# Kernel tuning notes

Measured on AMD Instinct MI355X. Metric: run time of the kernel, lower is better.

## Reference

```python
import jax, jax.numpy as jnp
import numpy as np

N = 50000   # nodes
E = 800000  # directed edges
IN, H1, H2, OUT = 128, 64, 32, 40
K = 2       # SGConv hops


def setup_inputs() -> dict:
    key = jax.random.key(0)
    ks = jax.random.split(key, 8)
    x = jax.random.normal(ks[0], (N, IN), dtype=jnp.float32)
    edge_index = jax.random.randint(ks[1], (2, E), 0, N, dtype=jnp.int64)
    s = lambda k, shp, fan: jax.random.normal(k, shp, dtype=jnp.float32) / np.sqrt(fan)
    return {
        "x": x,
        "edge_index": edge_index,
        "W1": s(ks[2], (IN, H1), IN), "b1": jnp.zeros((H1,), jnp.float32),
        "W2": s(ks[3], (H1, H2), H1), "b2": jnp.zeros((H2,), jnp.float32),
        "Wf": s(ks[4], (H2, OUT), H2), "bf": jnp.zeros((OUT,), jnp.float32),
    }


def _gcn_norm(edge_index, num_nodes):
    # add self-loops, then norm = d^{-1/2}[src] * d^{-1/2}[dst], d over targets
    loop = jnp.arange(num_nodes, dtype=edge_index.dtype)
    src = jnp.concatenate([edge_index[0], loop])
    dst = jnp.concatenate([edge_index[1], loop])
    deg = jax.ops.segment_sum(jnp.ones_like(src, dtype=jnp.float32), dst,
                              num_segments=num_nodes)
    dinv = jnp.where(deg > 0, jax.lax.rsqrt(deg), 0.0)
    norm = dinv[src] * dinv[dst]  # [E + N]
    return src, dst, norm


def _propagate_k(x, src, dst, norm, num_nodes, k):
    for _ in range(k):
        x = jax.ops.segment_sum(x[src] * norm[:, None], dst,
                                num_segments=num_nodes)
    return x


def reference(x, edge_index, W1, b1, W2, b2, Wf, bf):
    num_nodes = x.shape[0]
    src, dst, norm = _gcn_norm(edge_index, num_nodes)
    # SGConv layer 1: A_hat^K x, then linear, then relu
    h = _propagate_k(x, src, dst, norm, num_nodes, K)
    h = jax.nn.relu(h @ W1 + b1)
    # SGConv layer 2
    h = _propagate_k(h, src, dst, norm, num_nodes, K)
    h = jax.nn.relu(h @ W2 + b2)
    embedding = h
    logits = h @ Wf + bf
    return (embedding, logits)
```

## Files before the change

kernel.cpp:

```cpp
#include <hip/hip_runtime.h>

#define NN 50000
#define NE 800000
#define IN_F 128
#define H1_F 64
#define H2_F 32
#define OUT_F 40

#define BSH 7
#define NBKT 391
#define CAPA 4032
#define CHUNK 4096
#define NCH ((NE + CHUNK - 1) / CHUNK)
#define NGEMM ((NN + 63) / 64)

static inline int cdiv(int a, int b) { return (a + b - 1) / b; }

__device__ __forceinline__ unsigned pack_e(int s, int d) {
    return ((unsigned)(d >> BSH) << 23) | ((unsigned)s << 7) | (unsigned)(d & 127);
}

struct GemmLDS { float Xs[64][33]; float Wsh[32][64]; };
struct BinALDS { int hist[512]; int incl[512]; int runSt[512]; int lcur[512]; int baseSh[512];
                 unsigned stage[CHUNK]; };

__global__ __launch_bounds__(256)
void phase1_k(const float* __restrict__ x, const float* __restrict__ W1,
              const int* __restrict__ src, const int* __restrict__ dst,
              unsigned* __restrict__ pairs, int* __restrict__ gCursor,
              float* __restrict__ t_out) {
    __shared__ union { GemmLDS g; BinALDS a; } lds;
    const int t = threadIdx.x;

    if (blockIdx.x < NGEMM) {
        const int rowBase = blockIdx.x * 64;
        const int tc = t % 16;
        const int tr = t / 16;
        float acc[4][4];
        #pragma unroll
        for (int i = 0; i < 4; ++i)
            #pragma unroll
            for (int j = 0; j < 4; ++j) acc[i][j] = 0.0f;

        for (int k0 = 0; k0 < IN_F; k0 += 32) {
            for (int l = t; l < 64 * 8; l += 256) {
                int r  = l / 8;
                int kk = (l % 8) * 4;
                float4 v = make_float4(0.f, 0.f, 0.f, 0.f);
                int gr = rowBase + r;
                if (gr < NN) v = *reinterpret_cast<const float4*>(x + (size_t)gr * IN_F + k0 + kk);
                lds.g.Xs[r][kk + 0] = v.x; lds.g.Xs[r][kk + 1] = v.y;
                lds.g.Xs[r][kk + 2] = v.z; lds.g.Xs[r][kk + 3] = v.w;
            }
            for (int l = t; l < 32 * 16; l += 256) {
                int kk = l / 16;
                int c  = (l % 16) * 4;
                *reinterpret_cast<float4*>(&lds.g.Wsh[kk][c]) =
                    *reinterpret_cast<const float4*>(W1 + (size_t)(k0 + kk) * H1_F + c);
            }
            __syncthreads();
            #pragma unroll
            for (int kk = 0; kk < 32; ++kk) {
                float wv[4];
                *reinterpret_cast<float4*>(wv) =
                    *reinterpret_cast<const float4*>(&lds.g.Wsh[kk][tc * 4]);
                #pragma unroll
                for (int i = 0; i < 4; ++i) {
                    float a = lds.g.Xs[tr * 4 + i][kk];
                    acc[i][0] = fmaf(a, wv[0], acc[i][0]);
                    acc[i][1] = fmaf(a, wv[1], acc[i][1]);
                    acc[i][2] = fmaf(a, wv[2], acc[i][2]);
                    acc[i][3] = fmaf(a, wv[3], acc[i][3]);
                }
            }
            __syncthreads();
        }
        #pragma unroll
        for (int i = 0; i < 4; ++i) {
            int gr = rowBase + tr * 4 + i;
            if (gr < NN) {
                float4 v;
                v.x = acc[i][0]; v.y = acc[i][1]; v.z = acc[i][2]; v.w = acc[i][3];
                *reinterpret_cast<float4*>(t_out + (size_t)gr * H1_F + tc * 4) = v;
            }
        }
    } else {
        const int e0 = (blockIdx.x - NGEMM) * CHUNK;
        const int n = min(CHUNK, NE - e0);
        lds.a.hist[t] = 0; lds.a.hist[t + 256] = 0;
        __syncthreads();
        for (int i = t; i < n; i += 256) {
            int d = dst[e0 + i];
            atomicAdd(&lds.a.hist[d >> BSH], 1);
        }
        __syncthreads();
        lds.a.incl[t] = lds.a.hist[t]; lds.a.incl[t + 256] = lds.a.hist[t + 256];
        __syncthreads();
        for (int off = 1; off < 512; off <<= 1) {
            int v0 = (t >= off) ? lds.a.incl[t - off] : 0;
            int v1 = (t + 256 >= off) ? lds.a.incl[t + 256 - off] : 0;
            __syncthreads();
            lds.a.incl[t] += v0; lds.a.incl[t + 256] += v1;
            __syncthreads();
        }
        lds.a.runSt[t]       = lds.a.incl[t] - lds.a.hist[t];
        lds.a.runSt[t + 256] = lds.a.incl[t + 256] - lds.a.hist[t + 256];
        lds.a.lcur[t]        = lds.a.runSt[t];
        lds.a.lcur[t + 256]  = lds.a.runSt[t + 256];
        __syncthreads();
        for (int i = t; i < n; i += 256) {
            int s = src[e0 + i], d = dst[e0 + i];
            int b = d >> BSH;
            int p = atomicAdd(&lds.a.lcur[b], 1);
            lds.a.stage[p] = pack_e(s, d);
        }
        for (int b = t; b < NBKT; b += 256) {
            int c = lds.a.hist[b];
            lds.a.baseSh[b] = c ? atomicAdd(&gCursor[b], c) : 0;
        }
        __syncthreads();
        for (int i = t; i < n; i += 256) {
            unsigned p = lds.a.stage[i];
            int b = (int)(p >> 23);
            int gp = lds.a.baseSh[b] + (i - lds.a.runSt[b]);
            if (gp < CAPA) pairs[(size_t)b * CAPA + gp] = p;
        }
    }
}

__global__ __launch_bounds__(256)
void binB_k(const unsigned* __restrict__ pairs, const int* __restrict__ gCursor,
            int2* __restrict__ rowptr, float* __restrict__ dinv, int* __restrict__ csr) {
    const int b = blockIdx.x;
    const int nodeBase = b << BSH;
    const int nNodes = min(128, NN - nodeBase);
    int count = min(gCursor[b], CAPA);
    const int seg = b * CAPA;
    __shared__ int hist[128], incl[128], lcur[128];
    const int t = threadIdx.x;
    if (t < 128) hist[t] = 0;
    __syncthreads();
    const unsigned* bp = pairs + (size_t)b * CAPA;
    for (int i = t; i < count; i += 256) {
        atomicAdd(&hist[bp[i] & 127], 1);
    }
    __syncthreads();
    if (t < 128) incl[t] = hist[t];
    __syncthreads();
    for (int off = 1; off < 128; off <<= 1) {
        int v = (t < 128 && t >= off) ? incl[t - off] : 0;
        __syncthreads();
        if (t < 128) incl[t] += v;
        __syncthreads();
    }
    if (t < nNodes) {
        int e = seg + incl[t];
        rowptr[nodeBase + t] = make_int2(e - hist[t], e);
        dinv[nodeBase + t]   = rsqrtf((float)hist[t] + 1.0f);
        lcur[t] = e - hist[t];
    }
    __syncthreads();
    for (int i = t; i < count; i += 256) {
        unsigned p = bp[i];
        int pos = atomicAdd(&lcur[p & 127], 1);
        csr[pos] = (int)((p >> 7) & 0xFFFFu);
    }
}

__global__ __launch_bounds__(256)
void pull1_k(const float* __restrict__ in, const int* __restrict__ csr,
             const int2* __restrict__ rowptr, const float* __restrict__ dinv,
             float* __restrict__ out) {
    const int t = threadIdx.x;
    const int node = blockIdx.x * 16 + t / 16;
    const int col  = (t % 16) * 4;
    if (node >= NN) return;
    const int2 rp = rowptr[node];
    const float dd = dinv[node];
    float4 s4 = *reinterpret_cast<const float4*>(in + (size_t)node * 64 + col);
    float4 a0, a1, a2, a3;
    a0.x = dd * s4.x; a0.y = dd * s4.y; a0.z = dd * s4.z; a0.w = dd * s4.w;
    a1 = make_float4(0.f, 0.f, 0.f, 0.f);
    a2 = make_float4(0.f, 0.f, 0.f, 0.f);
    a3 = make_float4(0.f, 0.f, 0.f, 0.f);
    int k = rp.x;
    for (; k + 3 < rp.y; k += 4) {
        int s0 = csr[k], s1 = csr[k + 1], s2 = csr[k + 2], s3 = csr[k + 3];
        float w0 = dinv[s0], w1 = dinv[s1], w2 = dinv[s2], w3 = dinv[s3];
        float4 v0 = *reinterpret_cast<const float4*>(in + (size_t)s0 * 64 + col);
        float4 v1 = *reinterpret_cast<const float4*>(in + (size_t)s1 * 64 + col);
        float4 v2 = *reinterpret_cast<const float4*>(in + (size_t)s2 * 64 + col);
        float4 v3 = *reinterpret_cast<const float4*>(in + (size_t)s3 * 64 + col);
        a0.x = fmaf(w0, v0.x, a0.x); a0.y = fmaf(w0, v0.y, a0.y);
        a0.z = fmaf(w0, v0.z, a0.z); a0.w = fmaf(w0, v0.w, a0.w);
        a1.x = fmaf(w1, v1.x, a1.x); a1.y = fmaf(w1, v1.y, a1.y);
        a1.z = fmaf(w1, v1.z, a1.z); a1.w = fmaf(w1, v1.w, a1.w);
        a2.x = fmaf(w2, v2.x, a2.x); a2.y = fmaf(w2, v2.y, a2.y);
        a2.z = fmaf(w2, v2.z, a2.z); a2.w = fmaf(w2, v2.w, a2.w);
        a3.x = fmaf(w3, v3.x, a3.x); a3.y = fmaf(w3, v3.y, a3.y);
        a3.z = fmaf(w3, v3.z, a3.z); a3.w = fmaf(w3, v3.w, a3.w);
    }
    for (; k < rp.y; ++k) {
        int s0 = csr[k];
        float w0 = dinv[s0];
        float4 v0 = *reinterpret_cast<const float4*>(in + (size_t)s0 * 64 + col);
        a0.x = fmaf(w0, v0.x, a0.x); a0.y = fmaf(w0, v0.y, a0.y);
        a0.z = fmaf(w0, v0.z, a0.z); a0.w = fmaf(w0, v0.w, a0.w);
    }
    const float sc = dd * dd;
    float4 r;
    r.x = (a0.x + a1.x + a2.x + a3.x) * sc;
    r.y = (a0.y + a1.y + a2.y + a3.y) * sc;
    r.z = (a0.z + a1.z + a2.z + a3.z) * sc;
    r.w = (a0.w + a1.w + a2.w + a3.w) * sc;
    *reinterpret_cast<float4*>(out + (size_t)node * 64 + col) = r;
}

__global__ __launch_bounds__(256)
void pull32_k(const float* __restrict__ in, const int* __restrict__ csr,
              const int2* __restrict__ rowptr, const float* __restrict__ dinv,
              float* __restrict__ out) {
    const int t = threadIdx.x;
    const int node = blockIdx.x * 32 + t / 8;
    const int col  = (t % 8) * 4;
    if (node >= NN) return;
    const int2 rp = rowptr[node];
    float4 a0 = *reinterpret_cast<const float4*>(in + (size_t)node * 32 + col);
    float4 a1 = make_float4(0.f, 0.f, 0.f, 0.f);
    float4 a2 = make_float4(0.f, 0.f, 0.f, 0.f);
    float4 a3 = make_float4(0.f, 0.f, 0.f, 0.f);
    int k = rp.x;
    for (; k + 3 < rp.y; k += 4) {
        int s0 = csr[k], s1 = csr[k + 1], s2 = csr[k + 2], s3 = csr[k + 3];
        float4 v0 = *reinterpret_cast<const float4*>(in + (size_t)s0 * 32 + col);
        float4 v1 = *reinterpret_cast<const float4*>(in + (size_t)s1 * 32 + col);
        float4 v2 = *reinterpret_cast<const float4*>(in + (size_t)s2 * 32 + col);
        float4 v3 = *reinterpret_cast<const float4*>(in + (size_t)s3 * 32 + col);
        a0.x += v0.x; a0.y += v0.y; a0.z += v0.z; a0.w += v0.w;
        a1.x += v1.x; a1.y += v1.y; a1.z += v1.z; a1.w += v1.w;
        a2.x += v2.x; a2.y += v2.y; a2.z += v2.z; a2.w += v2.w;
        a3.x += v3.x; a3.y += v3.y; a3.z += v3.z; a3.w += v3.w;
    }
    for (; k < rp.y; ++k) {
        int s0 = csr[k];
        float4 v0 = *reinterpret_cast<const float4*>(in + (size_t)s0 * 32 + col);
        a0.x += v0.x; a0.y += v0.y; a0.z += v0.z; a0.w += v0.w;
    }
    float sc = dinv[node]; sc *= sc;
    float4 r;
    r.x = (a0.x + a1.x + a2.x + a3.x) * sc;
    r.y = (a0.y + a1.y + a2.y + a3.y) * sc;
    r.z = (a0.z + a1.z + a2.z + a3.z) * sc;
    r.w = (a0.w + a1.w + a2.w + a3.w) * sc;
    *reinterpret_cast<float4*>(out + (size_t)node * 32 + col) = r;
}

__global__ __launch_bounds__(256)
void pullgemm2_k(const float* __restrict__ in, const int* __restrict__ csr,
                 const int2* __restrict__ rowptr, const float* __restrict__ dinv,
                 const float* __restrict__ b1, const float* __restrict__ W2,
                 float* __restrict__ outT) {
    __shared__ float hs[64][68];
    __shared__ float W2s[64][32];
    const int t = threadIdx.x;
    for (int i = t; i < 64 * 32 / 4; i += 256)
        reinterpret_cast<float4*>(&W2s[0][0])[i] = reinterpret_cast<const float4*>(W2)[i];
    const int nodeBase = blockIdx.x * 64;
    #pragma unroll
    for (int pass = 0; pass < 4; ++pass) {
        const int nb = pass * 16 + t / 16;
        const int node = nodeBase + nb;
        const int col = (t % 16) * 4;
        float4 r = make_float4(0.f, 0.f, 0.f, 0.f);
        if (node < NN) {
            const int2 rp = rowptr[node];
            float4 a0 = *reinterpret_cast<const float4*>(in + (size_t)node * 64 + col);
            float4 a1 = make_float4(0.f, 0.f, 0.f, 0.f);
            float4 a2 = make_float4(0.f, 0.f, 0.f, 0.f);
            float4 a3 = make_float4(0.f, 0.f, 0.f, 0.f);
            int k = rp.x;
            for (; k + 3 < rp.y; k += 4) {
                int s0 = csr[k], s1 = csr[k + 1], s2 = csr[k + 2], s3 = csr[k + 3];
                float4 v0 = *reinterpret_cast<const float4*>(in + (size_t)s0 * 64 + col);
                float4 v1 = *reinterpret_cast<const float4*>(in + (size_t)s1 * 64 + col);
                float4 v2 = *reinterpret_cast<const float4*>(in + (size_t)s2 * 64 + col);
                float4 v3 = *reinterpret_cast<const float4*>(in + (size_t)s3 * 64 + col);
                a0.x += v0.x; a0.y += v0.y; a0.z += v0.z; a0.w += v0.w;
                a1.x += v1.x; a1.y += v1.y; a1.z += v1.z; a1.w += v1.w;
                a2.x += v2.x; a2.y += v2.y; a2.z += v2.z; a2.w += v2.w;
                a3.x += v3.x; a3.y += v3.y; a3.z += v3.z; a3.w += v3.w;
            }
            for (; k < rp.y; ++k) {
                int s0 = csr[k];
                float4 v0 = *reinterpret_cast<const float4*>(in + (size_t)s0 * 64 + col);
                a0.x += v0.x; a0.y += v0.y; a0.z += v0.z; a0.w += v0.w;
            }
            const float sc = dinv[node];
            const float4 bv = *reinterpret_cast<const float4*>(b1 + col);
            r.x = fmaxf((a0.x + a1.x + a2.x + a3.x) * sc + bv.x, 0.f);
            r.y = fmaxf((a0.y + a1.y + a2.y + a3.y) * sc + bv.y, 0.f);
            r.z = fmaxf((a0.z + a1.z + a2.z + a3.z) * sc + bv.z, 0.f);
            r.w = fmaxf((a0.w + a1.w + a2.w + a3.w) * sc + bv.w, 0.f);
        }
        *reinterpret_cast<float4*>(&hs[nb][col]) = r;
    }
    __syncthreads();
    const int r = t / 4;
    const int c0 = (t % 4) * 8;
    float acc[8];
    #pragma unroll
    for (int j = 0; j < 8; ++j) acc[j] = 0.f;
    #pragma unroll 4
    for (int k = 0; k < 64; k += 4) {
        float4 av = *reinterpret_cast<const float4*>(&hs[r][k]);
        #pragma unroll
        for (int kk = 0; kk < 4; ++kk) {
            float a = (&av.x)[kk];
            float4 w0 = *reinterpret_cast<const float4*>(&W2s[k + kk][c0]);
            float4 w1 = *reinterpret_cast<const float4*>(&W2s[k + kk][c0 + 4]);
            acc[0] = fmaf(a, w0.x, acc[0]); acc[1] = fmaf(a, w0.y, acc[1]);
            acc[2] = fmaf(a, w0.z, acc[2]); acc[3] = fmaf(a, w0.w, acc[3]);
            acc[4] = fmaf(a, w1.x, acc[4]); acc[5] = fmaf(a, w1.y, acc[5]);
            acc[6] = fmaf(a, w1.z, acc[6]); acc[7] = fmaf(a, w1.w, acc[7]);
        }
    }
    const int node = nodeBase + r;
    if (node < NN) {
        const float sc = dinv[node];
        float4 o0, o1;
        o0.x = acc[0] * sc; o0.y = acc[1] * sc; o0.z = acc[2] * sc; o0.w = acc[3] * sc;
        o1.x = acc[4] * sc; o1.y = acc[5] * sc; o1.z = acc[6] * sc; o1.w = acc[7] * sc;
        *reinterpret_cast<float4*>(outT + (size_t)node * 32 + c0)     = o0;
        *reinterpret_cast<float4*>(outT + (size_t)node * 32 + c0 + 4) = o1;
    }
}

__global__ __launch_bounds__(256)
void pullgemmF_k(const float* __restrict__ in, const int* __restrict__ csr,
                 const int2* __restrict__ rowptr, const float* __restrict__ dinv,
                 const float* __restrict__ b2, const float* __restrict__ Wf,
                 const float* __restrict__ bf, float* __restrict__ embOut,
                 float* __restrict__ logits) {
    __shared__ float es[64][36];
    __shared__ float Wfs[32][40];
    __shared__ float bfs[40];
    const int t = threadIdx.x;
    for (int i = t; i < 32 * 40 / 4; i += 256)
        reinterpret_cast<float4*>(&Wfs[0][0])[i] = reinterpret_cast<const float4*>(Wf)[i];
    if (t < 40) bfs[t] = bf[t];
    const int nodeBase = blockIdx.x * 64;
    #pragma unroll
    for (int pass = 0; pass < 2; ++pass) {
        const int nb = pass * 32 + t / 8;
        const int node = nodeBase + nb;
        const int col = (t % 8) * 4;
        float4 r = make_float4(0.f, 0.f, 0.f, 0.f);
        if (node < NN) {
            const int2 rp = rowptr[node];
            float4 a0 = *reinterpret_cast<const float4*>(in + (size_t)node * 32 + col);
            float4 a1 = make_float4(0.f, 0.f, 0.f, 0.f);
            float4 a2 = make_float4(0.f, 0.f, 0.f, 0.f);
            float4 a3 = make_float4(0.f, 0.f, 0.f, 0.f);
            int k = rp.x;
            for (; k + 3 < rp.y; k += 4) {
                int s0 = csr[k], s1 = csr[k + 1], s2 = csr[k + 2], s3 = csr[k + 3];
                float4 v0 = *reinterpret_cast<const float4*>(in + (size_t)s0 * 32 + col);
                float4 v1 = *reinterpret_cast<const float4*>(in + (size_t)s1 * 32 + col);
                float4 v2 = *reinterpret_cast<const float4*>(in + (size_t)s2 * 32 + col);
                float4 v3 = *reinterpret_cast<const float4*>(in + (size_t)s3 * 32 + col);
                a0.x += v0.x; a0.y += v0.y; a0.z += v0.z; a0.w += v0.w;
                a1.x += v1.x; a1.y += v1.y; a1.z += v1.z; a1.w += v1.w;
                a2.x += v2.x; a2.y += v2.y; a2.z += v2.z; a2.w += v2.w;
                a3.x += v3.x; a3.y += v3.y; a3.z += v3.z; a3.w += v3.w;
            }
            for (; k < rp.y; ++k) {
                int s0 = csr[k];
                float4 v0 = *reinterpret_cast<const float4*>(in + (size_t)s0 * 32 + col);
                a0.x += v0.x; a0.y += v0.y; a0.z += v0.z; a0.w += v0.w;
            }
            const float sc = dinv[node];
            const float4 bv = *reinterpret_cast<const float4*>(b2 + col);
            r.x = fmaxf((a0.x + a1.x + a2.x + a3.x) * sc + bv.x, 0.f);
            r.y = fmaxf((a0.y + a1.y + a2.y + a3.y) * sc + bv.y, 0.f);
            r.z = fmaxf((a0.z + a1.z + a2.z + a3.z) * sc + bv.z, 0.f);
            r.w = fmaxf((a0.w + a1.w + a2.w + a3.w) * sc + bv.w, 0.f);
            *reinterpret_cast<float4*>(embOut + (size_t)node * 32 + col) = r;
        }
        *reinterpret_cast<float4*>(&es[nb][col]) = r;
    }
    __syncthreads();
    const int r = t / 4;
    const int c0 = (t % 4) * 10;
    float acc[10];
    #pragma unroll
    for (int j = 0; j < 10; ++j) acc[j] = bfs[c0 + j];
    #pragma unroll 4
    for (int k = 0; k < 32; k += 4) {
        float4 av = *reinterpret_cast<const float4*>(&es[r][k]);
        #pragma unroll
        for (int kk = 0; kk < 4; ++kk) {
            float a = (&av.x)[kk];
            #pragma unroll
            for (int j = 0; j < 10; ++j)
                acc[j] = fmaf(a, Wfs[k + kk][c0 + j], acc[j]);
        }
    }
    const int node = nodeBase + r;
    if (node < NN) {
        float* lp = logits + (size_t)node * 40 + c0;
        #pragma unroll
        for (int j = 0; j < 10; j += 2) {
            float2 o; o.x = acc[j]; o.y = acc[j + 1];
            *reinterpret_cast<float2*>(lp + j) = o;
        }
    }
}

extern "C" void kernel_launch(void* const* d_in, const int* in_sizes, int n_in,
                              void* d_out, int out_size, void* d_ws, size_t ws_size,
                              hipStream_t stream) {
    const float* x  = (const float*)d_in[0];
    const int*   ei = (const int*)d_in[1];
    const float* W1 = (const float*)d_in[2];
    const float* b1 = (const float*)d_in[3];
    const float* W2 = (const float*)d_in[4];
    const float* b2 = (const float*)d_in[5];
    const float* Wf = (const float*)d_in[6];
    const float* bf = (const float*)d_in[7];

    float* out    = (float*)d_out;
    float* embOut = out;
    float* logits = out + (size_t)NN * H2_F;

    const int* src = ei;
    const int* dst = ei + NE;

    float* ws      = (float*)d_ws;
    float*    dinv   = ws;
    int2*     rowptr = (int2*)(ws + NN);
    int*      csr    = (int*)(rowptr + NN);
    int*      gCursor= csr + (size_t)NBKT * CAPA;
    float*    bufA   = (float*)(gCursor + 512);
    float*    bufB   = bufA + (size_t)NN * 64;
    unsigned* pairs  = (unsigned*)bufB;

    hipMemsetAsync(gCursor, 0, NBKT * sizeof(int), stream);
    phase1_k<<<NGEMM + NCH, 256, 0, stream>>>(x, W1, src, dst, pairs, gCursor, bufA);
    binB_k<<<NBKT, 256, 0, stream>>>(pairs, gCursor, rowptr, dinv, csr);

    pull1_k<<<cdiv(NN, 16), 256, 0, stream>>>(bufA, csr, rowptr, dinv, bufB);
    pullgemm2_k<<<cdiv(NN, 64), 256, 0, stream>>>(bufB, csr, rowptr, dinv, b1, W2, bufA);

    pull32_k<<<cdiv(NN, 32), 256, 0, stream>>>(bufA, csr, rowptr, dinv, bufB);
    pullgemmF_k<<<cdiv(NN, 64), 256, 0, stream>>>(bufB, csr, rowptr, dinv, b2, Wf, bf, embOut, logits);
}
```

Baseline: 252.7 us.

## Prescale first-layer features by dinv in binB and shrink pull-GEMM node tiles

```diff
diff --git a/kernel.cpp b/kernel.cpp
--- a/kernel.cpp
+++ b/kernel.cpp
@@ -130,13 +130,15 @@
 
 __global__ __launch_bounds__(256)
 void binB_k(const unsigned* __restrict__ pairs, const int* __restrict__ gCursor,
-            int2* __restrict__ rowptr, float* __restrict__ dinv, int* __restrict__ csr) {
+            int2* __restrict__ rowptr, float* __restrict__ dinv, int* __restrict__ csr,
+            float* __restrict__ t_rows) {
     const int b = blockIdx.x;
     const int nodeBase = b << BSH;
     const int nNodes = min(128, NN - nodeBase);
     int count = min(gCursor[b], CAPA);
     const int seg = b * CAPA;
     __shared__ int hist[128], incl[128], lcur[128];
+    __shared__ float dsh[128];
     const int t = threadIdx.x;
     if (t < 128) hist[t] = 0;
     __syncthreads();
@@ -156,7 +158,9 @@
     if (t < nNodes) {
         int e = seg + incl[t];
         rowptr[nodeBase + t] = make_int2(e - hist[t], e);
-        dinv[nodeBase + t]   = rsqrtf((float)hist[t] + 1.0f);
+        float dv = rsqrtf((float)hist[t] + 1.0f);
+        dinv[nodeBase + t] = dv;
+        dsh[t] = dv;
         lcur[t] = e - hist[t];
     }
     __syncthreads();
@@ -165,6 +169,15 @@
         int pos = atomicAdd(&lcur[p & 127], 1);
         csr[pos] = (int)((p >> 7) & 0xFFFFu);
     }
+    const int nF4 = nNodes * 16;
+    for (int i = t; i < nF4; i += 256) {
+        int n = i >> 4, c = i & 15;
+        float4* p = reinterpret_cast<float4*>(t_rows + (size_t)(nodeBase + n) * 64) + c;
+        float4 v = *p;
+        float s = dsh[n];
+        v.x *= s; v.y *= s; v.z *= s; v.w *= s;
+        *p = v;
+    }
 }
 
 __global__ __launch_bounds__(256)
@@ -176,38 +189,28 @@
     const int col  = (t % 16) * 4;
     if (node >= NN) return;
     const int2 rp = rowptr[node];
-    const float dd = dinv[node];
-    float4 s4 = *reinterpret_cast<const float4*>(in + (size_t)node * 64 + col);
-    float4 a0, a1, a2, a3;
-    a0.x = dd * s4.x; a0.y = dd * s4.y; a0.z = dd * s4.z; a0.w = dd * s4.w;
-    a1 = make_float4(0.f, 0.f, 0.f, 0.f);
-    a2 = make_float4(0.f, 0.f, 0.f, 0.f);
-    a3 = make_float4(0.f, 0.f, 0.f, 0.f);
+    float4 a0 = *reinterpret_cast<const float4*>(in + (size_t)node * 64 + col);
+    float4 a1 = make_float4(0.f, 0.f, 0.f, 0.f);
+    float4 a2 = make_float4(0.f, 0.f, 0.f, 0.f);
+    float4 a3 = make_float4(0.f, 0.f, 0.f, 0.f);
     int k = rp.x;
     for (; k + 3 < rp.y; k += 4) {
         int s0 = csr[k], s1 = csr[k + 1], s2 = csr[k + 2], s3 = csr[k + 3];
-        float w0 = dinv[s0], w1 = dinv[s1], w2 = dinv[s2], w3 = dinv[s3];
         float4 v0 = *reinterpret_cast<const float4*>(in + (size_t)s0 * 64 + col);
         float4 v1 = *reinterpret_cast<const float4*>(in + (size_t)s1 * 64 + col);
         float4 v2 = *reinterpret_cast<const float4*>(in + (size_t)s2 * 64 + col);
         float4 v3 = *reinterpret_cast<const float4*>(in + (size_t)s3 * 64 + col);
-        a0.x = fmaf(w0, v0.x, a0.x); a0.y = fmaf(w0, v0.y, a0.y);
-        a0.z = fmaf(w0, v0.z, a0.z); a0.w = fmaf(w0, v0.w, a0.w);
-        a1.x = fmaf(w1, v1.x, a1.x); a1.y = fmaf(w1, v1.y, a1.y);
-        a1.z = fmaf(w1, v1.z, a1.z); a1.w = fmaf(w1, v1.w, a1.w);
-        a2.x = fmaf(w2, v2.x, a2.x); a2.y = fmaf(w2, v2.y, a2.y);
-        a2.z = fmaf(w2, v2.z, a2.z); a2.w = fmaf(w2, v2.w, a2.w);
-        a3.x = fmaf(w3, v3.x, a3.x); a3.y = fmaf(w3, v3.y, a3.y);
-        a3.z = fmaf(w3, v3.z, a3.z); a3.w = fmaf(w3, v3.w, a3.w);
+        a0.x += v0.x; a0.y += v0.y; a0.z += v0.z; a0.w += v0.w;
+        a1.x += v1.x; a1.y += v1.y; a1.z += v1.z; a1.w += v1.w;
+        a2.x += v2.x; a2.y += v2.y; a2.z += v2.z; a2.w += v2.w;
+        a3.x += v3.x; a3.y += v3.y; a3.z += v3.z; a3.w += v3.w;
     }
     for (; k < rp.y; ++k) {
         int s0 = csr[k];
-        float w0 = dinv[s0];
         float4 v0 = *reinterpret_cast<const float4*>(in + (size_t)s0 * 64 + col);
-        a0.x = fmaf(w0, v0.x, a0.x); a0.y = fmaf(w0, v0.y, a0.y);
-        a0.z = fmaf(w0, v0.z, a0.z); a0.w = fmaf(w0, v0.w, a0.w);
-    }
-    const float sc = dd * dd;
+        a0.x += v0.x; a0.y += v0.y; a0.z += v0.z; a0.w += v0.w;
+    }
+    float sc = dinv[node]; sc *= sc;
     float4 r;
     r.x = (a0.x + a1.x + a2.x + a3.x) * sc;
     r.y = (a0.y + a1.y + a2.y + a3.y) * sc;
@@ -260,14 +263,14 @@
                  const int2* __restrict__ rowptr, const float* __restrict__ dinv,
                  const float* __restrict__ b1, const float* __restrict__ W2,
                  float* __restrict__ outT) {
-    __shared__ float hs[64][68];
+    __shared__ float hs[32][68];
     __shared__ float W2s[64][32];
     const int t = threadIdx.x;
     for (int i = t; i < 64 * 32 / 4; i += 256)
         reinterpret_cast<float4*>(&W2s[0][0])[i] = reinterpret_cast<const float4*>(W2)[i];
-    const int nodeBase = blockIdx.x * 64;
+    const int nodeBase = blockIdx.x * 32;
     #pragma unroll
-    for (int pass = 0; pass < 4; ++pass) {
+    for (int pass = 0; pass < 2; ++pass) {
         const int nb = pass * 16 + t / 16;
         const int node = nodeBase + nb;
         const int col = (t % 16) * 4;
@@ -305,33 +308,26 @@
         *reinterpret_cast<float4*>(&hs[nb][col]) = r;
     }
     __syncthreads();
-    const int r = t / 4;
-    const int c0 = (t % 4) * 8;
-    float acc[8];
-    #pragma unroll
-    for (int j = 0; j < 8; ++j) acc[j] = 0.f;
+    const int r = t / 8;
+    const int c0 = (t % 8) * 4;
+    float acc[4] = {0.f, 0.f, 0.f, 0.f};
     #pragma unroll 4
     for (int k = 0; k < 64; k += 4) {
         float4 av = *reinterpret_cast<const float4*>(&hs[r][k]);
         #pragma unroll
         for (int kk = 0; kk < 4; ++kk) {
             float a = (&av.x)[kk];
-            float4 w0 = *reinterpret_cast<const float4*>(&W2s[k + kk][c0]);
-            float4 w1 = *reinterpret_cast<const float4*>(&W2s[k + kk][c0 + 4]);
-            acc[0] = fmaf(a, w0.x, acc[0]); acc[1] = fmaf(a, w0.y, acc[1]);
-            acc[2] = fmaf(a, w0.z, acc[2]); acc[3] = fmaf(a, w0.w, acc[3]);
-            acc[4] = fmaf(a, w1.x, acc[4]); acc[5] = fmaf(a, w1.y, acc[5]);
-            acc[6] = fmaf(a, w1.z, acc[6]); acc[7] = fmaf(a, w1.w, acc[7]);
+            float4 w = *reinterpret_cast<const float4*>(&W2s[k + kk][c0]);
+            acc[0] = fmaf(a, w.x, acc[0]); acc[1] = fmaf(a, w.y, acc[1]);
+            acc[2] = fmaf(a, w.z, acc[2]); acc[3] = fmaf(a, w.w, acc[3]);
         }
     }
     const int node = nodeBase + r;
     if (node < NN) {
         const float sc = dinv[node];
-        float4 o0, o1;
-        o0.x = acc[0] * sc; o0.y = acc[1] * sc; o0.z = acc[2] * sc; o0.w = acc[3] * sc;
-        o1.x = acc[4] * sc; o1.y = acc[5] * sc; o1.z = acc[6] * sc; o1.w = acc[7] * sc;
-        *reinterpret_cast<float4*>(outT + (size_t)node * 32 + c0)     = o0;
-        *reinterpret_cast<float4*>(outT + (size_t)node * 32 + c0 + 4) = o1;
+        float4 o;
+        o.x = acc[0] * sc; o.y = acc[1] * sc; o.z = acc[2] * sc; o.w = acc[3] * sc;
+        *reinterpret_cast<float4*>(outT + (size_t)node * 32 + c0) = o;
     }
 }
 
@@ -341,17 +337,16 @@
                  const float* __restrict__ b2, const float* __restrict__ Wf,
                  const float* __restrict__ bf, float* __restrict__ embOut,
                  float* __restrict__ logits) {
-    __shared__ float es[64][36];
+    __shared__ float es[32][36];
     __shared__ float Wfs[32][40];
     __shared__ float bfs[40];
     const int t = threadIdx.x;
     for (int i = t; i < 32 * 40 / 4; i += 256)
         reinterpret_cast<float4*>(&Wfs[0][0])[i] = reinterpret_cast<const float4*>(Wf)[i];
     if (t < 40) bfs[t] = bf[t];
-    const int nodeBase = blockIdx.x * 64;
-    #pragma unroll
-    for (int pass = 0; pass < 2; ++pass) {
-        const int nb = pass * 32 + t / 8;
+    const int nodeBase = blockIdx.x * 32;
+    {
+        const int nb = t / 8;
         const int node = nodeBase + nb;
         const int col = (t % 8) * 4;
         float4 r = make_float4(0.f, 0.f, 0.f, 0.f);
@@ -389,11 +384,11 @@
         *reinterpret_cast<float4*>(&es[nb][col]) = r;
     }
     __syncthreads();
-    const int r = t / 4;
-    const int c0 = (t % 4) * 10;
-    float acc[10];
+    const int r = t / 8;
+    const int c0 = (t % 8) * 5;
+    float acc[5];
     #pragma unroll
-    for (int j = 0; j < 10; ++j) acc[j] = bfs[c0 + j];
+    for (int j = 0; j < 5; ++j) acc[j] = bfs[c0 + j];
     #pragma unroll 4
     for (int k = 0; k < 32; k += 4) {
         float4 av = *reinterpret_cast<const float4*>(&es[r][k]);
@@ -401,7 +396,7 @@
         for (int kk = 0; kk < 4; ++kk) {
             float a = (&av.x)[kk];
             #pragma unroll
-            for (int j = 0; j < 10; ++j)
+            for (int j = 0; j < 5; ++j)
                 acc[j] = fmaf(a, Wfs[k + kk][c0 + j], acc[j]);
         }
     }
@@ -409,10 +404,7 @@
     if (node < NN) {
         float* lp = logits + (size_t)node * 40 + c0;
         #pragma unroll
-        for (int j = 0; j < 10; j += 2) {
-            float2 o; o.x = acc[j]; o.y = acc[j + 1];
-            *reinterpret_cast<float2*>(lp + j) = o;
-        }
+        for (int j = 0; j < 5; ++j) lp[j] = acc[j];
     }
 }
 
@@ -446,11 +438,11 @@
 
     hipMemsetAsync(gCursor, 0, NBKT * sizeof(int), stream);
     phase1_k<<<NGEMM + NCH, 256, 0, stream>>>(x, W1, src, dst, pairs, gCursor, bufA);
-    binB_k<<<NBKT, 256, 0, stream>>>(pairs, gCursor, rowptr, dinv, csr);
+    binB_k<<<NBKT, 256, 0, stream>>>(pairs, gCursor, rowptr, dinv, csr, bufA);
 
     pull1_k<<<cdiv(NN, 16), 256, 0, stream>>>(bufA, csr, rowptr, dinv, bufB);
-    pullgemm2_k<<<cdiv(NN, 64), 256, 0, stream>>>(bufB, csr, rowptr, dinv, b1, W2, bufA);
+    pullgemm2_k<<<cdiv(NN, 32), 256, 0, stream>>>(bufB, csr, rowptr, dinv, b1, W2, bufA);
 
     pull32_k<<<cdiv(NN, 32), 256, 0, stream>>>(bufA, csr, rowptr, dinv, bufB);
-    pullgemmF_k<<<cdiv(NN, 64), 256, 0, stream>>>(bufB, csr, rowptr, dinv, b2, Wf, bf, embOut, logits);
-}
+    pullgemmF_k<<<cdiv(NN, 32), 256, 0, stream>>>(bufB, csr, rowptr, dinv, b2, Wf, bf, embOut, logits);
+}
```

Measured after the change: 255.2 us. About the same (+1.0%).

## Store features in column slabs, use 16-bit CSR indices, split pulls from GEMMs

Applied to the files above, without the earlier changes.

```diff
diff --git a/kernel.cpp b/kernel.cpp
--- a/kernel.cpp
+++ b/kernel.cpp
@@ -13,6 +13,9 @@
 #define CHUNK 4096
 #define NCH ((NE + CHUNK - 1) / CHUNK)
 #define NGEMM ((NN + 63) / 64)
+
+#define S64 ((size_t)NN * 8)
+#define S32 ((size_t)NN * 4)
 
 static inline int cdiv(int a, int b) { return (a + b - 1) / b; }
 
@@ -75,13 +78,15 @@
             }
             __syncthreads();
         }
+        const int slab = tc >> 1;
+        const int coff = (tc & 1) * 4;
         #pragma unroll
         for (int i = 0; i < 4; ++i) {
             int gr = rowBase + tr * 4 + i;
             if (gr < NN) {
                 float4 v;
                 v.x = acc[i][0]; v.y = acc[i][1]; v.z = acc[i][2]; v.w = acc[i][3];
-                *reinterpret_cast<float4*>(t_out + (size_t)gr * H1_F + tc * 4) = v;
+                *reinterpret_cast<float4*>(t_out + (size_t)slab * S64 + (size_t)gr * 8 + coff) = v;
             }
         }
     } else {
@@ -130,13 +135,15 @@
 
 __global__ __launch_bounds__(256)
 void binB_k(const unsigned* __restrict__ pairs, const int* __restrict__ gCursor,
-            int2* __restrict__ rowptr, float* __restrict__ dinv, int* __restrict__ csr) {
+            int2* __restrict__ rowptr, float* __restrict__ dinv,
+            unsigned short* __restrict__ csr16, float* __restrict__ t_rows) {
     const int b = blockIdx.x;
     const int nodeBase = b << BSH;
     const int nNodes = min(128, NN - nodeBase);
     int count = min(gCursor[b], CAPA);
     const int seg = b * CAPA;
     __shared__ int hist[128], incl[128], lcur[128];
+    __shared__ float dsh[128];
     const int t = threadIdx.x;
     if (t < 128) hist[t] = 0;
     __syncthreads();
@@ -156,86 +163,53 @@
     if (t < nNodes) {
         int e = seg + incl[t];
         rowptr[nodeBase + t] = make_int2(e - hist[t], e);
-        dinv[nodeBase + t]   = rsqrtf((float)hist[t] + 1.0f);
+        float dv = rsqrtf((float)hist[t] + 1.0f);
+        dinv[nodeBase + t] = dv;
+        dsh[t] = dv;
         lcur[t] = e - hist[t];
     }
     __syncthreads();
     for (int i = t; i < count; i += 256) {
         unsigned p = bp[i];
         int pos = atomicAdd(&lcur[p & 127], 1);
-        csr[pos] = (int)((p >> 7) & 0xFFFFu);
-    }
-}
-
-__global__ __launch_bounds__(256)
-void pull1_k(const float* __restrict__ in, const int* __restrict__ csr,
-             const int2* __restrict__ rowptr, const float* __restrict__ dinv,
-             float* __restrict__ out) {
-    const int t = threadIdx.x;
-    const int node = blockIdx.x * 16 + t / 16;
-    const int col  = (t % 16) * 4;
+        csr16[pos] = (unsigned short)((p >> 7) & 0xFFFFu);
+    }
+    for (int s = 0; s < 8; ++s) {
+        for (int i = t; i < nNodes * 2; i += 256) {
+            int n = i >> 1, c4 = (i & 1) * 4;
+            float4* p = reinterpret_cast<float4*>(
+                t_rows + (size_t)s * S64 + (size_t)(nodeBase + n) * 8 + c4);
+            float4 v = *p;
+            float sc = dsh[n];
+            v.x *= sc; v.y *= sc; v.z *= sc; v.w *= sc;
+            *p = v;
+        }
+    }
+}
+
+template<bool EPI>
+__global__ __launch_bounds__(256)
+void pull64s_k(const float* __restrict__ in, const unsigned short* __restrict__ csr,
+               const int2* __restrict__ rowptr, const float* __restrict__ dinv,
+               const float* __restrict__ bias, float* __restrict__ out) {
+    const int t = threadIdx.x;
+    const int slab = blockIdx.x & 7;
+    const int node = ((blockIdx.x >> 3) << 7) + (t >> 1);
+    const int col  = (t & 1) * 4;
     if (node >= NN) return;
+    const float* sin = in + (size_t)slab * S64;
     const int2 rp = rowptr[node];
-    const float dd = dinv[node];
-    float4 s4 = *reinterpret_cast<const float4*>(in + (size_t)node * 64 + col);
-    float4 a0, a1, a2, a3;
-    a0.x = dd * s4.x; a0.y = dd * s4.y; a0.z = dd * s4.z; a0.w = dd * s4.w;
-    a1 = make_float4(0.f, 0.f, 0.f, 0.f);
-    a2 = make_float4(0.f, 0.f, 0.f, 0.f);
-    a3 = make_float4(0.f, 0.f, 0.f, 0.f);
-    int k = rp.x;
-    for (; k + 3 < rp.y; k += 4) {
-        int s0 = csr[k], s1 = csr[k + 1], s2 = csr[k + 2], s3 = csr[k + 3];
-        float w0 = dinv[s0], w1 = dinv[s1], w2 = dinv[s2], w3 = dinv[s3];
-        float4 v0 = *reinterpret_cast<const float4*>(in + (size_t)s0 * 64 + col);
-        float4 v1 = *reinterpret_cast<const float4*>(in + (size_t)s1 * 64 + col);
-        float4 v2 = *reinterpret_cast<const float4*>(in + (size_t)s2 * 64 + col);
-        float4 v3 = *reinterpret_cast<const float4*>(in + (size_t)s3 * 64 + col);
-        a0.x = fmaf(w0, v0.x, a0.x); a0.y = fmaf(w0, v0.y, a0.y);
-        a0.z = fmaf(w0, v0.z, a0.z); a0.w = fmaf(w0, v0.w, a0.w);
-        a1.x = fmaf(w1, v1.x, a1.x); a1.y = fmaf(w1, v1.y, a1.y);
-        a1.z = fmaf(w1, v1.z, a1.z); a1.w = fmaf(w1, v1.w, a1.w);
-        a2.x = fmaf(w2, v2.x, a2.x); a2.y = fmaf(w2, v2.y, a2.y);
-        a2.z = fmaf(w2, v2.z, a2.z); a2.w = fmaf(w2, v2.w, a2.w);
-        a3.x = fmaf(w3, v3.x, a3.x); a3.y = fmaf(w3, v3.y, a3.y);
-        a3.z = fmaf(w3, v3.z, a3.z); a3.w = fmaf(w3, v3.w, a3.w);
-    }
-    for (; k < rp.y; ++k) {
-        int s0 = csr[k];
-        float w0 = dinv[s0];
-        float4 v0 = *reinterpret_cast<const float4*>(in + (size_t)s0 * 64 + col);
-        a0.x = fmaf(w0, v0.x, a0.x); a0.y = fmaf(w0, v0.y, a0.y);
-        a0.z = fmaf(w0, v0.z, a0.z); a0.w = fmaf(w0, v0.w, a0.w);
-    }
-    const float sc = dd * dd;
-    float4 r;
-    r.x = (a0.x + a1.x + a2.x + a3.x) * sc;
-    r.y = (a0.y + a1.y + a2.y + a3.y) * sc;
-    r.z = (a0.z + a1.z + a2.z + a3.z) * sc;
-    r.w = (a0.w + a1.w + a2.w + a3.w) * sc;
-    *reinterpret_cast<float4*>(out + (size_t)node * 64 + col) = r;
-}
-
-__global__ __launch_bounds__(256)
-void pull32_k(const float* __restrict__ in, const int* __restrict__ csr,
-              const int2* __restrict__ rowptr, const float* __restrict__ dinv,
-              float* __restrict__ out) {
-    const int t = threadIdx.x;
-    const int node = blockIdx.x * 32 + t / 8;
-    const int col  = (t % 8) * 4;
-    if (node >= NN) return;
-    const int2 rp = rowptr[node];
-    float4 a0 = *reinterpret_cast<const float4*>(in + (size_t)node * 32 + col);
+    float4 a0 = *reinterpret_cast<const float4*>(sin + (size_t)node * 8 + col);
     float4 a1 = make_float4(0.f, 0.f, 0.f, 0.f);
     float4 a2 = make_float4(0.f, 0.f, 0.f, 0.f);
     float4 a3 = make_float4(0.f, 0.f, 0.f, 0.f);
     int k = rp.x;
     for (; k + 3 < rp.y; k += 4) {
         int s0 = csr[k], s1 = csr[k + 1], s2 = csr[k + 2], s3 = csr[k + 3];
-        float4 v0 = *reinterpret_cast<const float4*>(in + (size_t)s0 * 32 + col);
-        float4 v1 = *reinterpret_cast<const float4*>(in + (size_t)s1 * 32 + col);
-        float4 v2 = *reinterpret_cast<const float4*>(in + (size_t)s2 * 32 + col);
-        float4 v3 = *reinterpret_cast<const float4*>(in + (size_t)s3 * 32 + col);
+        float4 v0 = *reinterpret_cast<const float4*>(sin + (size_t)s0 * 8 + col);
+        float4 v1 = *reinterpret_cast<const float4*>(sin + (size_t)s1 * 8 + col);
+        float4 v2 = *reinterpret_cast<const float4*>(sin + (size_t)s2 * 8 + col);
+        float4 v3 = *reinterpret_cast<const float4*>(sin + (size_t)s3 * 8 + col);
         a0.x += v0.x; a0.y += v0.y; a0.z += v0.z; a0.w += v0.w;
         a1.x += v1.x; a1.y += v1.y; a1.z += v1.z; a1.w += v1.w;
         a2.x += v2.x; a2.y += v2.y; a2.z += v2.z; a2.w += v2.w;
@@ -243,70 +217,98 @@
     }
     for (; k < rp.y; ++k) {
         int s0 = csr[k];
-        float4 v0 = *reinterpret_cast<const float4*>(in + (size_t)s0 * 32 + col);
+        float4 v0 = *reinterpret_cast<const float4*>(sin + (size_t)s0 * 8 + col);
         a0.x += v0.x; a0.y += v0.y; a0.z += v0.z; a0.w += v0.w;
     }
-    float sc = dinv[node]; sc *= sc;
+    float dd = dinv[node];
     float4 r;
-    r.x = (a0.x + a1.x + a2.x + a3.x) * sc;
-    r.y = (a0.y + a1.y + a2.y + a3.y) * sc;
-    r.z = (a0.z + a1.z + a2.z + a3.z) * sc;
-    r.w = (a0.w + a1.w + a2.w + a3.w) * sc;
-    *reinterpret_cast<float4*>(out + (size_t)node * 32 + col) = r;
-}
-
-__global__ __launch_bounds__(256)
-void pullgemm2_k(const float* __restrict__ in, const int* __restrict__ csr,
-                 const int2* __restrict__ rowptr, const float* __restrict__ dinv,
-                 const float* __restrict__ b1, const float* __restrict__ W2,
-                 float* __restrict__ outT) {
+    if (EPI) {
+        const float4 bv = *reinterpret_cast<const float4*>(bias + slab * 8 + col);
+        r.x = fmaxf((a0.x + a1.x + a2.x + a3.x) * dd + bv.x, 0.f);
+        r.y = fmaxf((a0.y + a1.y + a2.y + a3.y) * dd + bv.y, 0.f);
+        r.z = fmaxf((a0.z + a1.z + a2.z + a3.z) * dd + bv.z, 0.f);
+        r.w = fmaxf((a0.w + a1.w + a2.w + a3.w) * dd + bv.w, 0.f);
+    } else {
+        float sc = dd * dd;
+        r.x = (a0.x + a1.x + a2.x + a3.x) * sc;
+        r.y = (a0.y + a1.y + a2.y + a3.y) * sc;
+        r.z = (a0.z + a1.z + a2.z + a3.z) * sc;
+        r.w = (a0.w + a1.w + a2.w + a3.w) * sc;
+    }
+    *reinterpret_cast<float4*>(out + (size_t)slab * S64 + (size_t)node * 8 + col) = r;
+}
+
+template<bool EPI>
+__global__ __launch_bounds__(256)
+void pull32s_k(const float* __restrict__ in, const unsigned short* __restrict__ csr,
+               const int2* __restrict__ rowptr, const float* __restrict__ dinv,
+               const float* __restrict__ bias, float* __restrict__ out) {
+    const int t = threadIdx.x;
+    const int slab = blockIdx.x & 7;
+    const int node = ((blockIdx.x >> 3) << 8) + t;
+    if (node >= NN) return;
+    const float* sin = in + (size_t)slab * S32;
+    const int2 rp = rowptr[node];
+    float4 a0 = *reinterpret_cast<const float4*>(sin + (size_t)node * 4);
+    float4 a1 = make_float4(0.f, 0.f, 0.f, 0.f);
+    float4 a2 = make_float4(0.f, 0.f, 0.f, 0.f);
+    float4 a3 = make_float4(0.f, 0.f, 0.f, 0.f);
+    int k = rp.x;
+    for (; k + 3 < rp.y; k += 4) {
+        int s0 = csr[k], s1 = csr[k + 1], s2 = csr[k + 2], s3 = csr[k + 3];
+        float4 v0 = *reinterpret_cast<const float4*>(sin + (size_t)s0 * 4);
+        float4 v1 = *reinterpret_cast<const float4*>(sin + (size_t)s1 * 4);
+        float4 v2 = *reinterpret_cast<const float4*>(sin + (size_t)s2 * 4);
+        float4 v3 = *reinterpret_cast<const float4*>(sin + (size_t)s3 * 4);
+        a0.x += v0.x; a0.y += v0.y; a0.z += v0.z; a0.w += v0.w;
+        a1.x += v1.x; a1.y += v1.y; a1.z += v1.z; a1.w += v1.w;
+        a2.x += v2.x; a2.y += v2.y; a2.z += v2.z; a2.w += v2.w;
+        a3.x += v3.x; a3.y += v3.y; a3.z += v3.z; a3.w += v3.w;
+    }
+    for (; k < rp.y; ++k) {
+        int s0 = csr[k];
+        float4 v0 = *reinterpret_cast<const float4*>(sin + (size_t)s0 * 4);
+        a0.x += v0.x; a0.y += v0.y; a0.z += v0.z; a0.w += v0.w;
+    }
+    float dd = dinv[node];
+    float4 r;
+    if (EPI) {
+        const float4 bv = *reinterpret_cast<const float4*>(bias + slab * 4);
+        r.x = fmaxf((a0.x + a1.x + a2.x + a3.x) * dd + bv.x, 0.f);
+        r.y = fmaxf((a0.y + a1.y + a2.y + a3.y) * dd + bv.y, 0.f);
+        r.z = fmaxf((a0.z + a1.z + a2.z + a3.z) * dd + bv.z, 0.f);
+        r.w = fmaxf((a0.w + a1.w + a2.w + a3.w) * dd + bv.w, 0.f);
+    } else {
+        float sc = dd * dd;
+        r.x = (a0.x + a1.x + a2.x + a3.x) * sc;
+        r.y = (a0.y + a1.y + a2.y + a3.y) * sc;
+        r.z = (a0.z + a1.z + a2.z + a3.z) * sc;
+        r.w = (a0.w + a1.w + a2.w + a3.w) * sc;
+    }
+    *reinterpret_cast<float4*>(out + (size_t)slab * S32 + (size_t)node * 4) = r;
+}
+
+__global__ __launch_bounds__(256)
+void gemm2_k(const float* __restrict__ h, const float* __restrict__ W2,
+             const float* __restrict__ dinv, float* __restrict__ t2) {
     __shared__ float hs[64][68];
     __shared__ float W2s[64][32];
     const int t = threadIdx.x;
+    const int n0 = blockIdx.x * 64;
     for (int i = t; i < 64 * 32 / 4; i += 256)
         reinterpret_cast<float4*>(&W2s[0][0])[i] = reinterpret_cast<const float4*>(W2)[i];
-    const int nodeBase = blockIdx.x * 64;
-    #pragma unroll
-    for (int pass = 0; pass < 4; ++pass) {
-        const int nb = pass * 16 + t / 16;
-        const int node = nodeBase + nb;
-        const int col = (t % 16) * 4;
-        float4 r = make_float4(0.f, 0.f, 0.f, 0.f);
-        if (node < NN) {
-            const int2 rp = rowptr[node];
-            float4 a0 = *reinterpret_cast<const float4*>(in + (size_t)node * 64 + col);
-            float4 a1 = make_float4(0.f, 0.f, 0.f, 0.f);
-            float4 a2 = make_float4(0.f, 0.f, 0.f, 0.f);
-            float4 a3 = make_float4(0.f, 0.f, 0.f, 0.f);
-            int k = rp.x;
-            for (; k + 3 < rp.y; k += 4) {
-                int s0 = csr[k], s1 = csr[k + 1], s2 = csr[k + 2], s3 = csr[k + 3];
-                float4 v0 = *reinterpret_cast<const float4*>(in + (size_t)s0 * 64 + col);
-                float4 v1 = *reinterpret_cast<const float4*>(in + (size_t)s1 * 64 + col);
-                float4 v2 = *reinterpret_cast<const float4*>(in + (size_t)s2 * 64 + col);
-                float4 v3 = *reinterpret_cast<const float4*>(in + (size_t)s3 * 64 + col);
-                a0.x += v0.x; a0.y += v0.y; a0.z += v0.z; a0.w += v0.w;
-                a1.x += v1.x; a1.y += v1.y; a1.z += v1.z; a1.w += v1.w;
-                a2.x += v2.x; a2.y += v2.y; a2.z += v2.z; a2.w += v2.w;
-                a3.x += v3.x; a3.y += v3.y; a3.z += v3.z; a3.w += v3.w;
-            }
-            for (; k < rp.y; ++k) {
-                int s0 = csr[k];
-                float4 v0 = *reinterpret_cast<const float4*>(in + (size_t)s0 * 64 + col);
-                a0.x += v0.x; a0.y += v0.y; a0.z += v0.z; a0.w += v0.w;
-            }
-            const float sc = dinv[node];
-            const float4 bv = *reinterpret_cast<const float4*>(b1 + col);
-            r.x = fmaxf((a0.x + a1.x + a2.x + a3.x) * sc + bv.x, 0.f);
-            r.y = fmaxf((a0.y + a1.y + a2.y + a3.y) * sc + bv.y, 0.f);
-            r.z = fmaxf((a0.z + a1.z + a2.z + a3.z) * sc + bv.z, 0.f);
-            r.w = fmaxf((a0.w + a1.w + a2.w + a3.w) * sc + bv.w, 0.f);
-        }
-        *reinterpret_cast<float4*>(&hs[nb][col]) = r;
-    }
-    __syncthreads();
-    const int r = t / 4;
-    const int c0 = (t % 4) * 8;
+    for (int idx = t; idx < 1024; idx += 256) {
+        int s = idx >> 7;
+        int r = (idx >> 1) & 63;
+        int c2 = (idx & 1) * 4;
+        int node = n0 + r;
+        float4 v = make_float4(0.f, 0.f, 0.f, 0.f);
+        if (node < NN) v = *reinterpret_cast<const float4*>(h + (size_t)s * S64 + (size_t)node * 8 + c2);
+        *reinterpret_cast<float4*>(&hs[r][s * 8 + c2]) = v;
+    }
+    __syncthreads();
+    const int r = t >> 2;
+    const int c0 = (t & 3) * 8;
     float acc[8];
     #pragma unroll
     for (int j = 0; j < 8; ++j) acc[j] = 0.f;
@@ -324,73 +326,49 @@
             acc[6] = fmaf(a, w1.z, acc[6]); acc[7] = fmaf(a, w1.w, acc[7]);
         }
     }
-    const int node = nodeBase + r;
+    const int node = n0 + r;
     if (node < NN) {
         const float sc = dinv[node];
         float4 o0, o1;
         o0.x = acc[0] * sc; o0.y = acc[1] * sc; o0.z = acc[2] * sc; o0.w = acc[3] * sc;
         o1.x = acc[4] * sc; o1.y = acc[5] * sc; o1.z = acc[6] * sc; o1.w = acc[7] * sc;
-        *reinterpret_cast<float4*>(outT + (size_t)node * 32 + c0)     = o0;
-        *reinterpret_cast<float4*>(outT + (size_t)node * 32 + c0 + 4) = o1;
-    }
-}
-
-__global__ __launch_bounds__(256)
-void pullgemmF_k(const float* __restrict__ in, const int* __restrict__ csr,
-                 const int2* __restrict__ rowptr, const float* __restrict__ dinv,
-                 const float* __restrict__ b2, const float* __restrict__ Wf,
-                 const float* __restrict__ bf, float* __restrict__ embOut,
-                 float* __restrict__ logits) {
+        const int s0 = c0 >> 2;
+        *reinterpret_cast<float4*>(t2 + (size_t)s0 * S32 + (size_t)node * 4)       = o0;
+        *reinterpret_cast<float4*>(t2 + (size_t)(s0 + 1) * S32 + (size_t)node * 4) = o1;
+    }
+}
+
+__global__ __launch_bounds__(256)
+void gemmF_k(const float* __restrict__ e, const float* __restrict__ Wf,
+             const float* __restrict__ bf, float* __restrict__ embOut,
+             float* __restrict__ logits) {
     __shared__ float es[64][36];
     __shared__ float Wfs[32][40];
     __shared__ float bfs[40];
     const int t = threadIdx.x;
+    const int n0 = blockIdx.x * 64;
     for (int i = t; i < 32 * 40 / 4; i += 256)
         reinterpret_cast<float4*>(&Wfs[0][0])[i] = reinterpret_cast<const float4*>(Wf)[i];
     if (t < 40) bfs[t] = bf[t];
-    const int nodeBase = blockIdx.x * 64;
-    #pragma unroll
-    for (int pass = 0; pass < 2; ++pass) {
-        const int nb = pass * 32 + t / 8;
-        const int node = nodeBase + nb;
-        const int col = (t % 8) * 4;
-        float4 r = make_float4(0.f, 0.f, 0.f, 0.f);
-        if (node < NN) {
-            const int2 rp = rowptr[node];
-            float4 a0 = *reinterpret_cast<const float4*>(in + (size_t)node * 32 + col);
-            float4 a1 = make_float4(0.f, 0.f, 0.f, 0.f);
-            float4 a2 = make_float4(0.f, 0.f, 0.f, 0.f);
-            float4 a3 = make_float4(0.f, 0.f, 0.f, 0.f);
-            int k = rp.x;
-            for (; k + 3 < rp.y; k += 4) {
-                int s0 = csr[k], s1 = csr[k + 1], s2 = csr[k + 2], s3 = csr[k + 3];
-                float4 v0 = *reinterpret_cast<const float4*>(in + (size_t)s0 * 32 + col);
-                float4 v1 = *reinterpret_cast<const float4*>(in + (size_t)s1 * 32 + col);
-                float4 v2 = *reinterpret_cast<const float4*>(in + (size_t)s2 * 32 + col);
-                float4 v3 = *reinterpret_cast<const float4*>(in + (size_t)s3 * 32 + col);
-                a0.x += v0.x; a0.y += v0.y; a0.z += v0.z; a0.w += v0.w;
-                a1.x += v1.x; a1.y += v1.y; a1.z += v1.z; a1.w += v1.w;
-                a2.x += v2.x; a2.y += v2.y; a2.z += v2.z; a2.w += v2.w;
-                a3.x += v3.x; a3.y += v3.y; a3.z += v3.z; a3.w += v3.w;
-            }
-            for (; k < rp.y; ++k) {
-                int s0 = csr[k];
-                float4 v0 = *reinterpret_cast<const float4*>(in + (size_t)s0 * 32 + col);
-                a0.x += v0.x; a0.y += v0.y; a0.z += v0.z; a0.w += v0.w;
-            }
-            const float sc = dinv[node];
-            const float4 bv = *reinterpret_cast<const float4*>(b2 + col);
-            r.x = fmaxf((a0.x + a1.x + a2.x + a3.x) * sc + bv.x, 0.f);
-            r.y = fmaxf((a0.y + a1.y + a2.y + a3.y) * sc + bv.y, 0.f);
-            r.z = fmaxf((a0.z + a1.z + a2.z + a3.z) * sc + bv.z, 0.f);
-            r.w = fmaxf((a0.w + a1.w + a2.w + a3.w) * sc + bv.w, 0.f);
-            *reinterpret_cast<float4*>(embOut + (size_t)node * 32 + col) = r;
-        }
-        *reinterpret_cast<float4*>(&es[nb][col]) = r;
-    }
-    __syncthreads();
-    const int r = t / 4;
-    const int c0 = (t % 4) * 10;
+    for (int idx = t; idx < 512; idx += 256) {
+        int s = idx >> 6;
+        int r = idx & 63;
+        int node = n0 + r;
+        float4 v = make_float4(0.f, 0.f, 0.f, 0.f);
+        if (node < NN) v = *reinterpret_cast<const float4*>(e + (size_t)s * S32 + (size_t)node * 4);
+        *reinterpret_cast<float4*>(&es[r][s * 4]) = v;
+    }
+    __syncthreads();
+    for (int idx = t; idx < 512; idx += 256) {
+        int r = idx >> 3;
+        int c4 = (idx & 7) * 4;
+        int node = n0 + r;
+        if (node < NN)
+            *reinterpret_cast<float4*>(embOut + (size_t)node * 32 + c4) =
+                *reinterpret_cast<const float4*>(&es[r][c4]);
+    }
+    const int r = t >> 2;
+    const int c0 = (t & 3) * 10;
     float acc[10];
     #pragma unroll
     for (int j = 0; j < 10; ++j) acc[j] = bfs[c0 + j];
@@ -405,14 +383,11 @@
                 acc[j] = fmaf(a, Wfs[k + kk][c0 + j], acc[j]);
         }
     }
-    const int node = nodeBase + r;
+    const int node = n0 + r;
     if (node < NN) {
         float* lp = logits + (size_t)node * 40 + c0;
         #pragma unroll
-        for (int j = 0; j < 10; j += 2) {
-            float2 o; o.x = acc[j]; o.y = acc[j + 1];
-            *reinterpret_cast<float2*>(lp + j) = o;
-        }
+        for (int j = 0; j < 10; ++j) lp[j] = acc[j];
     }
 }
 
@@ -435,22 +410,24 @@
     const int* src = ei;
     const int* dst = ei + NE;
 
-    float* ws      = (float*)d_ws;
-    float*    dinv   = ws;
-    int2*     rowptr = (int2*)(ws + NN);
-    int*      csr    = (int*)(rowptr + NN);
-    int*      gCursor= csr + (size_t)NBKT * CAPA;
-    float*    bufA   = (float*)(gCursor + 512);
-    float*    bufB   = bufA + (size_t)NN * 64;
-    unsigned* pairs  = (unsigned*)bufB;
+    float* ws = (float*)d_ws;
+    float*          dinv   = ws;
+    int2*           rowptr = (int2*)(ws + NN);
+    unsigned short* csr16  = (unsigned short*)(rowptr + NN);
+    int*            gCursor= (int*)((char*)csr16 + (size_t)NBKT * CAPA * 2);
+    float*          bufA   = (float*)(gCursor + 512);
+    float*          bufB   = bufA + 8 * S64;
+    unsigned*       pairs  = (unsigned*)bufB;
 
     hipMemsetAsync(gCursor, 0, NBKT * sizeof(int), stream);
     phase1_k<<<NGEMM + NCH, 256, 0, stream>>>(x, W1, src, dst, pairs, gCursor, bufA);
-    binB_k<<<NBKT, 256, 0, stream>>>(pairs, gCursor, rowptr, dinv, csr);
-
-    pull1_k<<<cdiv(NN, 16), 256, 0, stream>>>(bufA, csr, rowptr, dinv, bufB);
-    pullgemm2_k<<<cdiv(NN, 64), 256, 0, stream>>>(bufB, csr, rowptr, dinv, b1, W2, bufA);
-
-    pull32_k<<<cdiv(NN, 32), 256, 0, stream>>>(bufA, csr, rowptr, dinv, bufB);
-    pullgemmF_k<<<cdiv(NN, 64), 256, 0, stream>>>(bufB, csr, rowptr, dinv, b2, Wf, bf, embOut, logits);
-}
+    binB_k<<<NBKT, 256, 0, stream>>>(pairs, gCursor, rowptr, dinv, csr16, bufA);
+
+    pull64s_k<false><<<8 * cdiv(NN, 128), 256, 0, stream>>>(bufA, csr16, rowptr, dinv, nullptr, bufB);
+    pull64s_k<true> <<<8 * cdiv(NN, 128), 256, 0, stream>>>(bufB, csr16, rowptr, dinv, b1, bufA);
+    gemm2_k<<<cdiv(NN, 64), 256, 0, stream>>>(bufA, W2, dinv, bufB);
+
+    pull32s_k<false><<<8 * cdiv(NN, 256), 256, 0, stream>>>(bufB, csr16, rowptr, dinv, nullptr, bufA);
+    pull32s_k<true> <<<8 * cdiv(NN, 256), 256, 0, stream>>>(bufA, csr16, rowptr, dinv, b2, bufB);
+    gemmF_k<<<cdiv(NN, 64), 256, 0, stream>>>(bufB, Wf, bf, embOut, logits);
+}
```

After: 294.4 us. 1.17x slower.
